# Optimization experiments

Measured on AMD Instinct MI355X. Metric: run time of the kernel, lower is better.

The kernel has to match this reference:

```python
import jax, jax.numpy as jnp
import numpy as np

TAU = 32.0
ALPHA = 0.9
B, C, F = 4096, 512, 128  # batch, n_classes, n_bits


def setup_inputs() -> dict:
    key = jax.random.key(0)
    k1, k2, k3, k4 = jax.random.split(key, 4)
    X = jax.random.normal(k1, (B, F), dtype=jnp.float32)
    T = jax.random.randint(k2, (B, C), 0, 2).astype(jnp.int32)  # 0/1 multi-label
    # kaiming_normal_(mode='fan_out') on a [C, F] tensor -> std = sqrt(2 / C)
    std = np.sqrt(2.0 / C).astype(np.float32)
    means = jax.random.normal(k3, (C, F), dtype=jnp.float32) * std
    log_vars = jax.random.normal(k4, (C, F), dtype=jnp.float32) * std
    return {"X": X, "T": T, "means": means, "log_vars": log_vars}


def _l2_normalize(x, eps=1e-12):
    # matches torch F.normalize(p=2): x / max(||x||, eps)
    n = jnp.sqrt(jnp.sum(x * x, axis=-1, keepdims=True))
    return x / jnp.maximum(n, eps)


def _mahalanobis(Xn, mu, log_vars):
    # M[i,j] = sum_f (x_if - mu_jf)^2 / exp(lv_jf)
    # expanded into three GEMM-like terms -> never materializes [N,C,F]
    inv = jnp.exp(-log_vars)                         # [C, F]
    t1 = (Xn * Xn) @ inv.T                           # [N, C]
    t2 = Xn @ (mu * inv).T                           # [N, C]
    t3 = jnp.sum(mu * mu * inv, axis=-1)             # [C]
    return t1 - 2.0 * t2 + t3[None, :]


def reference(X, T, means, log_vars):
    lv = jnp.clip(log_vars, 0.0, 6.0)                # relu6
    Xn = _l2_normalize(X)
    mu = _l2_normalize(means)
    D = _mahalanobis(Xn, mu, lv)                     # [N, C]

    P_all = jax.nn.softmax(-TAU * D, axis=1)         # [N, C]
    Tf = T.astype(X.dtype)
    P_sum = jnp.sum(P_all * Tf, axis=1)              # [N]
    nz = P_sum != 0
    safe = jnp.where(nz, P_sum, 1.0)
    loss = -jnp.sum(jnp.where(nz, jnp.log(safe), 0.0)) / jnp.maximum(
        jnp.sum(nz).astype(X.dtype), 1.0)

    # classes present in the batch (concrete mask -> static column selection)
    cw = np.asarray(jnp.sum(T, axis=0) != 0)
    Dc = D[:, cw]                                    # [N, Ccw]
    Tc = Tf[:, cw]
    S = Tc + jnp.exp(-ALPHA * Dc) * (1.0 - Tc)
    return (loss, S)
```

## Files before the change

kernel.cpp:

```cpp
#include <hip/hip_runtime.h>
#include <hip/hip_bf16.h>
#include <math.h>

#define NB 4096
#define NC 512
#define NF 128
#define NK 256
#define TAUc 32.0f
#define ALPHAc 0.9f

typedef __attribute__((ext_vector_type(8))) short bf16x8;
typedef __attribute__((ext_vector_type(4))) float f32x4;

__device__ inline void splitbf(float x, short& hi, short& lo) {
  unsigned u = __float_as_uint(x);
  hi = (short)(u >> 16);
  float l = x - __uint_as_float(u & 0xFFFF0000u);
  lo = (short)(__float_as_uint(l) >> 16);
}

__global__ __launch_bounds__(128) void k_prepB(const float* __restrict__ means,
                                               const float* __restrict__ logv,
                                               ushort* __restrict__ Bh,
                                               ushort* __restrict__ Bl,
                                               float* __restrict__ t3) {
  __shared__ float p2[2];
  __shared__ float q2[2];
  int c = blockIdx.x, f = threadIdx.x;
  float mu = means[(size_t)c * NF + f];
  float lv = fminf(fmaxf(logv[(size_t)c * NF + f], 0.f), 6.f);
  float iv = __expf(-lv);
  float s = mu * mu;
  #pragma unroll
  for (int o = 1; o < 64; o <<= 1) s += __shfl_xor(s, o, 64);
  if ((f & 63) == 0) p2[f >> 6] = s;
  __syncthreads();
  float mun = mu / fmaxf(sqrtf(p2[0] + p2[1]), 1e-12f);

  int ct = c >> 4, lr = c & 15;
  auto swadr = [&](int k) {
    return (size_t)(ct * 8 + (k >> 5)) * 512 + ((k >> 3) & 3) * 128 + lr * 8 + (k & 7);
  };
  short h, l;
  splitbf(iv, h, l);
  size_t a1 = swadr(f);
  Bh[a1] = (ushort)h; Bl[a1] = (ushort)l;
  splitbf(-2.f * mun * iv, h, l);
  size_t a2 = swadr(f + NF);
  Bh[a2] = (ushort)h; Bl[a2] = (ushort)l;

  float t = mun * mun * iv;
  #pragma unroll
  for (int o = 1; o < 64; o <<= 1) t += __shfl_xor(t, o, 64);
  if ((f & 63) == 0) q2[f >> 6] = t;
  __syncthreads();
  if (f == 0) t3[c] = q2[0] + q2[1];
}

__global__ __launch_bounds__(512) void k_zero(int* __restrict__ colnz) {
  colnz[threadIdx.x] = 0;
}

__global__ __launch_bounds__(256) void k_mask(const int* __restrict__ T,
                                              int* __restrict__ colnz) {
  int r0 = blockIdx.x * 16;
  int a0 = 0, a1 = 0;
  for (int r = 0; r < 16; ++r) {
    const int* row = T + (size_t)(r0 + r) * NC;
    a0 |= row[threadIdx.x];
    a1 |= row[threadIdx.x + 256];
  }
  if (a0) atomicOr(colnz + threadIdx.x, 1);
  if (a1) atomicOr(colnz + threadIdx.x + 256, 1);
}

__global__ __launch_bounds__(512) void k_scan(const int* __restrict__ colnz,
                                              int* __restrict__ pos) {
  __shared__ int s[NC];
  int t = threadIdx.x;
  int f = colnz[t] ? 1 : 0;
  s[t] = f;
  __syncthreads();
  for (int o = 1; o < NC; o <<= 1) {
    int add = (t >= o) ? s[t - o] : 0;
    __syncthreads();
    s[t] += add;
    __syncthreads();
  }
  pos[t] = s[t] - f;
}

__global__ __launch_bounds__(512) void k_fused(const float* __restrict__ X,
                                               const int* __restrict__ T,
                                               const ushort* __restrict__ Bh,
                                               const ushort* __restrict__ Bl,
                                               const float* __restrict__ t3,
                                               const int* __restrict__ colnz,
                                               const int* __restrict__ pos,
                                               float* __restrict__ Sout,
                                               float* __restrict__ blklog,
                                               int* __restrict__ blkcnt,
                                               int Csel, int ident) {
  __shared__ float Dls[16][514];
  __shared__ float sl16[16];
  __shared__ int sc16[16];
  int tid = threadIdx.x;
  int lane = tid & 63, w = tid >> 6;
  int lr = lane & 15, kq = lane >> 4;
  int r0 = blockIdx.x * 16;

  float xv[4][8];
  float rsum = 0.f;
  const float* xrow = X + (size_t)(r0 + lr) * NF + 8 * kq;
  #pragma unroll
  for (int c = 0; c < 4; ++c) {
    float4 u0 = *(const float4*)(xrow + 32 * c);
    float4 u1 = *(const float4*)(xrow + 32 * c + 4);
    xv[c][0] = u0.x; xv[c][1] = u0.y; xv[c][2] = u0.z; xv[c][3] = u0.w;
    xv[c][4] = u1.x; xv[c][5] = u1.y; xv[c][6] = u1.z; xv[c][7] = u1.w;
    #pragma unroll
    for (int j = 0; j < 8; ++j) rsum = fmaf(xv[c][j], xv[c][j], rsum);
  }
  rsum += __shfl_xor(rsum, 16, 64);
  rsum += __shfl_xor(rsum, 32, 64);
  float rn = 1.0f / fmaxf(sqrtf(rsum), 1e-12f);

  bf16x8 Afh[8], Afl[8];
  #pragma unroll
  for (int c = 0; c < 4; ++c) {
    #pragma unroll
    for (int j = 0; j < 8; ++j) {
      float xn = xv[c][j] * rn;
      short h, l;
      splitbf(xn * xn, h, l);
      Afh[c][j] = h; Afl[c][j] = l;
      splitbf(xn, h, l);
      Afh[c + 4][j] = h; Afl[c + 4][j] = l;
    }
  }

  int tf0[8], tf1[8];
  {
    const int* Trow0 = T + (size_t)(r0 + 2 * w) * NC;
    const int* Trow1 = T + (size_t)(r0 + 2 * w + 1) * NC;
    #pragma unroll
    for (int j = 0; j < 8; ++j) {
      tf0[j] = Trow0[lane + 64 * j];
      tf1[j] = Trow1[lane + 64 * j];
    }
  }

  f32x4 acc[4] = {};
  #pragma unroll
  for (int k8 = 0; k8 < 8; ++k8) {
    #pragma unroll
    for (int t = 0; t < 4; ++t) {
      size_t off = (((size_t)(w * 4 + t) * 8 + k8) * 64 + lane) * 8;
      bf16x8 bh = *(const bf16x8*)(Bh + off);
      bf16x8 bl = *(const bf16x8*)(Bl + off);
      acc[t] = __builtin_amdgcn_mfma_f32_16x16x32_bf16(Afh[k8], bh, acc[t], 0, 0, 0);
      acc[t] = __builtin_amdgcn_mfma_f32_16x16x32_bf16(Afl[k8], bh, acc[t], 0, 0, 0);
      acc[t] = __builtin_amdgcn_mfma_f32_16x16x32_bf16(Afh[k8], bl, acc[t], 0, 0, 0);
    }
  }

  int n0 = w * 64;
  #pragma unroll
  for (int t = 0; t < 4; ++t) {
    int c = n0 + 16 * t + lr;
    float tt = t3[c];
    #pragma unroll
    for (int i = 0; i < 4; ++i) Dls[4 * kq + i][c] = acc[t][i] + tt;
  }
  __syncthreads();

  #pragma unroll
  for (int rr = 0; rr < 2; ++rr) {
    int r = 2 * w + rr;
    const int* tf = rr ? tf1 : tf0;
    float d[8];
    #pragma unroll
    for (int j = 0; j < 8; ++j) d[j] = Dls[r][lane + 64 * j];
    float dmin = d[0];
    #pragma unroll
    for (int j = 1; j < 8; ++j) dmin = fminf(dmin, d[j]);
    #pragma unroll
    for (int o = 1; o < 64; o <<= 1) dmin = fminf(dmin, __shfl_xor(dmin, o, 64));
    float Z = 0.f, Ps = 0.f;
    #pragma unroll
    for (int j = 0; j < 8; ++j) {
      float p = __expf(TAUc * (dmin - d[j]));
      Z += p;
      if (tf[j]) Ps += p;
    }
    #pragma unroll
    for (int o = 1; o < 64; o <<= 1) { Z += __shfl_xor(Z, o, 64); Ps += __shfl_xor(Ps, o, 64); }
    float* srow = Sout + (size_t)(r0 + r) * Csel;
    if (ident) {
      #pragma unroll
      for (int j = 0; j < 8; ++j)
        srow[lane + 64 * j] = tf[j] ? 1.0f : __expf(-ALPHAc * d[j]);
    } else {
      #pragma unroll
      for (int j = 0; j < 8; ++j) {
        int c = lane + 64 * j;
        if (colnz[c]) srow[pos[c]] = tf[j] ? 1.0f : __expf(-ALPHAc * d[j]);
      }
    }
    if (lane == 0) {
      float Psum = Ps / Z;
      sl16[r] = (Psum > 0.f) ? logf(Psum) : 0.f;
      sc16[r] = (Psum > 0.f) ? 1 : 0;
    }
  }
  __syncthreads();
  if (tid == 0) {
    float s = 0.f; int c = 0;
    #pragma unroll
    for (int r = 0; r < 16; ++r) { s += sl16[r]; c += sc16[r]; }
    blklog[blockIdx.x] = s;
    blkcnt[blockIdx.x] = c;
  }
}

__global__ __launch_bounds__(256) void k_fin(const float* __restrict__ blklog,
                                             const int* __restrict__ blkcnt,
                                             float* __restrict__ out) {
  __shared__ float sl[256];
  __shared__ int sc[256];
  int t = threadIdx.x;
  sl[t] = blklog[t];
  sc[t] = blkcnt[t];
  __syncthreads();
  for (int o = 128; o > 0; o >>= 1) {
    if (t < o) { sl[t] += sl[t + o]; sc[t] += sc[t + o]; }
    __syncthreads();
  }
  if (t == 0) out[0] = -sl[0] / fmaxf((float)sc[0], 1.0f);
}

extern "C" void kernel_launch(void* const* d_in, const int* in_sizes, int n_in,
                              void* d_out, int out_size, void* d_ws, size_t ws_size,
                              hipStream_t stream) {
  const float* X     = (const float*)d_in[0];
  const int*   T     = (const int*)d_in[1];
  const float* means = (const float*)d_in[2];
  const float* logv  = (const float*)d_in[3];
  float* out = (float*)d_out;
  char* ws = (char*)d_ws;

  ushort* Bh      = (ushort*)(ws);
  ushort* Bl      = (ushort*)(ws + 262144);
  float*  t3      = (float*) (ws + 524288);
  float*  blklog  = (float*) (ws + 526336);
  int*    blkcnt  = (int*)   (ws + 527360);
  int*    colnz   = (int*)   (ws + 528384);
  int*    pos     = (int*)   (ws + 530432);

  int Csel = (out_size - 1) / NB;
  int ident = (Csel == NC);

  k_prepB<<<NC, NF, 0, stream>>>(means, logv, Bh, Bl, t3);
  if (!ident) {
    k_zero<<<1, NC, 0, stream>>>(colnz);
    k_mask<<<NB / 16, 256, 0, stream>>>(T, colnz);
    k_scan<<<1, NC, 0, stream>>>(colnz, pos);
  }
  k_fused<<<NB / 16, 512, 0, stream>>>(X, T, Bh, Bl, t3, colnz, pos,
                                       out + 1, blklog, blkcnt, Csel, ident);
  k_fin<<<1, 256, 0, stream>>>(blklog, blkcnt, out);
}
```

Measured before the change: 25.52 us.

## Double-buffer B fragments into LDS with async global_load_lds prefetch

Each wave now streams its hi/lo B fragments for the next K step into a private double-buffered LDS region using async global-to-LDS loads. It then reads the current step's fragments from LDS for the MFMAs. The goal is to overlap global memory latency with the matrix-core work instead of stalling on register loads each iteration. The shared buffer is enlarged to 128KB and reused for the D tile after a barrier. This limits blocks per CU and relies on hand-placed vmcnt waits, with no explicit guard against overwriting a buffer before its LDS reads finish.

```diff
diff --git a/kernel.cpp b/kernel.cpp
--- a/kernel.cpp
+++ b/kernel.cpp
@@ -11,6 +11,8 @@
 
 typedef __attribute__((ext_vector_type(8))) short bf16x8;
 typedef __attribute__((ext_vector_type(4))) float f32x4;
+typedef __attribute__((address_space(1))) const unsigned int gu32;
+typedef __attribute__((address_space(3))) unsigned int lu32;
 
 __device__ inline void splitbf(float x, short& hi, short& lo) {
   unsigned u = __float_as_uint(x);
@@ -101,13 +103,25 @@
                                                float* __restrict__ blklog,
                                                int* __restrict__ blkcnt,
                                                int Csel, int ident) {
-  __shared__ float Dls[16][514];
+  __shared__ __align__(16) unsigned char smraw[131072];
   __shared__ float sl16[16];
   __shared__ int sc16[16];
   int tid = threadIdx.x;
   int lane = tid & 63, w = tid >> 6;
   int lr = lane & 15, kq = lane >> 4;
   int r0 = blockIdx.x * 16;
+
+  auto stage = [&](int p) {
+    int par = p & 1;
+    #pragma unroll
+    for (int t = 0; t < 4; ++t) {
+      size_t goff = (((size_t)(w * 4 + t) * 8 + p) * 64 + lane) * 8;
+      unsigned ldso = (unsigned)(w * 16384 + par * 8192 + t * 2048);
+      __builtin_amdgcn_global_load_lds((gu32*)(Bh + goff), (lu32*)(smraw + ldso), 16, 0, 0);
+      __builtin_amdgcn_global_load_lds((gu32*)(Bl + goff), (lu32*)(smraw + ldso + 1024), 16, 0, 0);
+    }
+  };
+  stage(0);
 
   float xv[4][8];
   float rsum = 0.f;
@@ -150,20 +164,29 @@
     }
   }
 
+  const bf16x8* wstage = (const bf16x8*)(smraw + w * 16384);
   f32x4 acc[4] = {};
   #pragma unroll
   for (int k8 = 0; k8 < 8; ++k8) {
+    if (k8 < 7) {
+      stage(k8 + 1);
+      asm volatile("s_waitcnt vmcnt(8)" ::: "memory");
+    } else {
+      asm volatile("s_waitcnt vmcnt(0)" ::: "memory");
+    }
+    int par = k8 & 1;
     #pragma unroll
     for (int t = 0; t < 4; ++t) {
-      size_t off = (((size_t)(w * 4 + t) * 8 + k8) * 64 + lane) * 8;
-      bf16x8 bh = *(const bf16x8*)(Bh + off);
-      bf16x8 bl = *(const bf16x8*)(Bl + off);
+      bf16x8 bh = wstage[(par * 8 + t * 2) * 64 + lane];
+      bf16x8 bl = wstage[(par * 8 + t * 2 + 1) * 64 + lane];
       acc[t] = __builtin_amdgcn_mfma_f32_16x16x32_bf16(Afh[k8], bh, acc[t], 0, 0, 0);
       acc[t] = __builtin_amdgcn_mfma_f32_16x16x32_bf16(Afl[k8], bh, acc[t], 0, 0, 0);
       acc[t] = __builtin_amdgcn_mfma_f32_16x16x32_bf16(Afh[k8], bl, acc[t], 0, 0, 0);
     }
   }
-
+  __syncthreads();
+
+  float (*Dls)[514] = (float (*)[514])smraw;
   int n0 = w * 64;
   #pragma unroll
   for (int t = 0; t < 4; ++t) {
```

Result: faster. 23.75 us (-6.9%).

## Retile fused kernel to 64x128 blocks with B staged in LDS and split softmax

Applied to the files above, without the earlier changes.

Each block now handles a 64-row by 128-class tile instead of 16 full rows. The B operand slice (hi and lo bf16) is staged once into 128KB of LDS via global_load_lds, so each block reads it from memory once instead of every wave loading it from global. Softmax statistics are computed per column-chunk as partial min, Z and P values, merged per row across the 4 chunks in k_fin with online-softmax rescaling. This removes redundant B reads and the Dls shared-memory transpose. The cost is a large LDS footprint that limits occupancy to one block per CU, plus extra partial-statistic traffic.

```diff
diff --git a/kernel.cpp b/kernel.cpp
--- a/kernel.cpp
+++ b/kernel.cpp
@@ -11,6 +11,8 @@
 
 typedef __attribute__((ext_vector_type(8))) short bf16x8;
 typedef __attribute__((ext_vector_type(4))) float f32x4;
+typedef __attribute__((address_space(1))) const unsigned int gu32;
+typedef __attribute__((address_space(3))) unsigned int lu32;
 
 __device__ inline void splitbf(float x, short& hi, short& lo) {
   unsigned u = __float_as_uint(x);
@@ -98,145 +100,187 @@
                                                const int* __restrict__ colnz,
                                                const int* __restrict__ pos,
                                                float* __restrict__ Sout,
-                                               float* __restrict__ blklog,
-                                               int* __restrict__ blkcnt,
+                                               float* __restrict__ rowm,
+                                               float* __restrict__ rowz,
+                                               float* __restrict__ rowp,
                                                int Csel, int ident) {
-  __shared__ float Dls[16][514];
-  __shared__ float sl16[16];
-  __shared__ int sc16[16];
+  __shared__ __align__(16) unsigned char smB[131072];
+  __shared__ float partm[2][64], partz[2][64], partp[2][64];
   int tid = threadIdx.x;
   int lane = tid & 63, w = tid >> 6;
+  int wm = w & 3, wn = w >> 2;
   int lr = lane & 15, kq = lane >> 4;
-  int r0 = blockIdx.x * 16;
-
-  float xv[4][8];
-  float rsum = 0.f;
-  const float* xrow = X + (size_t)(r0 + lr) * NF + 8 * kq;
-  #pragma unroll
-  for (int c = 0; c < 4; ++c) {
-    float4 u0 = *(const float4*)(xrow + 32 * c);
-    float4 u1 = *(const float4*)(xrow + 32 * c + 4);
-    xv[c][0] = u0.x; xv[c][1] = u0.y; xv[c][2] = u0.z; xv[c][3] = u0.w;
-    xv[c][4] = u1.x; xv[c][5] = u1.y; xv[c][6] = u1.z; xv[c][7] = u1.w;
-    #pragma unroll
-    for (int j = 0; j < 8; ++j) rsum = fmaf(xv[c][j], xv[c][j], rsum);
-  }
-  rsum += __shfl_xor(rsum, 16, 64);
-  rsum += __shfl_xor(rsum, 32, 64);
-  float rn = 1.0f / fmaxf(sqrtf(rsum), 1e-12f);
+  int bx = blockIdx.x;
+  int gc = bx & 3, gr = bx >> 2;
+  int r0 = gr * 64, c0 = gc * 128;
+
+  {
+    const ushort* gh = Bh + (size_t)gc * 32768;
+    const ushort* gl = Bl + (size_t)gc * 32768;
+    #pragma unroll
+    for (int s = 0; s < 8; ++s) {
+      unsigned lo = (unsigned)(s * 8192 + w * 1024);
+      size_t ge = (size_t)(s * 512 + w * 64 + lane) * 8;
+      __builtin_amdgcn_global_load_lds((gu32*)(gh + ge), (lu32*)(smB + lo), 16, 0, 0);
+      __builtin_amdgcn_global_load_lds((gu32*)(gl + ge), (lu32*)(smB + 65536 + lo), 16, 0, 0);
+    }
+  }
 
   bf16x8 Afh[8], Afl[8];
-  #pragma unroll
-  for (int c = 0; c < 4; ++c) {
-    #pragma unroll
-    for (int j = 0; j < 8; ++j) {
-      float xn = xv[c][j] * rn;
-      short h, l;
-      splitbf(xn * xn, h, l);
-      Afh[c][j] = h; Afl[c][j] = l;
-      splitbf(xn, h, l);
-      Afh[c + 4][j] = h; Afl[c + 4][j] = l;
-    }
-  }
-
-  int tf0[8], tf1[8];
   {
-    const int* Trow0 = T + (size_t)(r0 + 2 * w) * NC;
-    const int* Trow1 = T + (size_t)(r0 + 2 * w + 1) * NC;
-    #pragma unroll
-    for (int j = 0; j < 8; ++j) {
-      tf0[j] = Trow0[lane + 64 * j];
-      tf1[j] = Trow1[lane + 64 * j];
-    }
-  }
+    float xv[4][8];
+    float rsum = 0.f;
+    const float* xrow = X + (size_t)(r0 + wm * 16 + lr) * NF + 8 * kq;
+    #pragma unroll
+    for (int c = 0; c < 4; ++c) {
+      float4 u0 = *(const float4*)(xrow + 32 * c);
+      float4 u1 = *(const float4*)(xrow + 32 * c + 4);
+      xv[c][0] = u0.x; xv[c][1] = u0.y; xv[c][2] = u0.z; xv[c][3] = u0.w;
+      xv[c][4] = u1.x; xv[c][5] = u1.y; xv[c][6] = u1.z; xv[c][7] = u1.w;
+      #pragma unroll
+      for (int j = 0; j < 8; ++j) rsum = fmaf(xv[c][j], xv[c][j], rsum);
+    }
+    rsum += __shfl_xor(rsum, 16, 64);
+    rsum += __shfl_xor(rsum, 32, 64);
+    float rn = 1.0f / fmaxf(sqrtf(rsum), 1e-12f);
+    #pragma unroll
+    for (int c = 0; c < 4; ++c) {
+      #pragma unroll
+      for (int j = 0; j < 8; ++j) {
+        float xn = xv[c][j] * rn;
+        short h, l;
+        splitbf(xn * xn, h, l);
+        Afh[c][j] = h; Afl[c][j] = l;
+        splitbf(xn, h, l);
+        Afh[c + 4][j] = h; Afl[c + 4][j] = l;
+      }
+    }
+  }
+
+  int tfv[4][4];
+  #pragma unroll
+  for (int i = 0; i < 4; ++i) {
+    const int* tr = T + (size_t)(r0 + wm * 16 + 4 * kq + i) * NC + c0 + wn * 64 + lr;
+    #pragma unroll
+    for (int t = 0; t < 4; ++t) tfv[t][i] = tr[16 * t];
+  }
+
+  __syncthreads();
 
   f32x4 acc[4] = {};
   #pragma unroll
   for (int k8 = 0; k8 < 8; ++k8) {
     #pragma unroll
     for (int t = 0; t < 4; ++t) {
-      size_t off = (((size_t)(w * 4 + t) * 8 + k8) * 64 + lane) * 8;
-      bf16x8 bh = *(const bf16x8*)(Bh + off);
-      bf16x8 bl = *(const bf16x8*)(Bl + off);
+      unsigned off = (unsigned)((((wn * 4 + t) * 8 + k8) * 64 + lane) * 16);
+      bf16x8 bh = *(const bf16x8*)(smB + off);
+      bf16x8 bl = *(const bf16x8*)(smB + 65536 + off);
       acc[t] = __builtin_amdgcn_mfma_f32_16x16x32_bf16(Afh[k8], bh, acc[t], 0, 0, 0);
       acc[t] = __builtin_amdgcn_mfma_f32_16x16x32_bf16(Afl[k8], bh, acc[t], 0, 0, 0);
       acc[t] = __builtin_amdgcn_mfma_f32_16x16x32_bf16(Afh[k8], bl, acc[t], 0, 0, 0);
     }
   }
 
-  int n0 = w * 64;
+  float d[4][4];
   #pragma unroll
   for (int t = 0; t < 4; ++t) {
-    int c = n0 + 16 * t + lr;
-    float tt = t3[c];
-    #pragma unroll
-    for (int i = 0; i < 4; ++i) Dls[4 * kq + i][c] = acc[t][i] + tt;
-  }
-  __syncthreads();
-
-  #pragma unroll
-  for (int rr = 0; rr < 2; ++rr) {
-    int r = 2 * w + rr;
-    const int* tf = rr ? tf1 : tf0;
-    float d[8];
-    #pragma unroll
-    for (int j = 0; j < 8; ++j) d[j] = Dls[r][lane + 64 * j];
-    float dmin = d[0];
-    #pragma unroll
-    for (int j = 1; j < 8; ++j) dmin = fminf(dmin, d[j]);
-    #pragma unroll
-    for (int o = 1; o < 64; o <<= 1) dmin = fminf(dmin, __shfl_xor(dmin, o, 64));
-    float Z = 0.f, Ps = 0.f;
-    #pragma unroll
-    for (int j = 0; j < 8; ++j) {
-      float p = __expf(TAUc * (dmin - d[j]));
+    float tt = t3[c0 + wn * 64 + 16 * t + lr];
+    #pragma unroll
+    for (int i = 0; i < 4; ++i) d[t][i] = acc[t][i] + tt;
+  }
+
+  float m4[4], Zi[4], Pi[4];
+  #pragma unroll
+  for (int i = 0; i < 4; ++i) {
+    float mm = fminf(fminf(d[0][i], d[1][i]), fminf(d[2][i], d[3][i]));
+    #pragma unroll
+    for (int o = 1; o < 16; o <<= 1) mm = fminf(mm, __shfl_xor(mm, o, 64));
+    float Z = 0.f, P = 0.f;
+    #pragma unroll
+    for (int t = 0; t < 4; ++t) {
+      float p = __expf(TAUc * (mm - d[t][i]));
       Z += p;
-      if (tf[j]) Ps += p;
-    }
-    #pragma unroll
-    for (int o = 1; o < 64; o <<= 1) { Z += __shfl_xor(Z, o, 64); Ps += __shfl_xor(Ps, o, 64); }
-    float* srow = Sout + (size_t)(r0 + r) * Csel;
-    if (ident) {
+      if (tfv[t][i]) P += p;
+    }
+    #pragma unroll
+    for (int o = 1; o < 16; o <<= 1) { Z += __shfl_xor(Z, o, 64); P += __shfl_xor(P, o, 64); }
+    m4[i] = mm; Zi[i] = Z; Pi[i] = P;
+  }
+
+  if (ident) {
+    #pragma unroll
+    for (int i = 0; i < 4; ++i) {
+      float* srow = Sout + (size_t)(r0 + wm * 16 + 4 * kq + i) * NC + c0 + wn * 64 + lr;
       #pragma unroll
-      for (int j = 0; j < 8; ++j)
-        srow[lane + 64 * j] = tf[j] ? 1.0f : __expf(-ALPHAc * d[j]);
-    } else {
+      for (int t = 0; t < 4; ++t)
+        srow[16 * t] = tfv[t][i] ? 1.0f : __expf(-ALPHAc * d[t][i]);
+    }
+  } else {
+    #pragma unroll
+    for (int i = 0; i < 4; ++i) {
+      float* srow = Sout + (size_t)(r0 + wm * 16 + 4 * kq + i) * Csel;
       #pragma unroll
-      for (int j = 0; j < 8; ++j) {
-        int c = lane + 64 * j;
-        if (colnz[c]) srow[pos[c]] = tf[j] ? 1.0f : __expf(-ALPHAc * d[j]);
+      for (int t = 0; t < 4; ++t) {
+        int c = c0 + wn * 64 + 16 * t + lr;
+        if (colnz[c]) srow[pos[c]] = tfv[t][i] ? 1.0f : __expf(-ALPHAc * d[t][i]);
       }
     }
-    if (lane == 0) {
-      float Psum = Ps / Z;
-      sl16[r] = (Psum > 0.f) ? logf(Psum) : 0.f;
-      sc16[r] = (Psum > 0.f) ? 1 : 0;
-    }
-  }
+  }
+
+  if (lr == 0) {
+    #pragma unroll
+    for (int i = 0; i < 4; ++i) {
+      int row = wm * 16 + 4 * kq + i;
+      partm[wn][row] = m4[i];
+      partz[wn][row] = Zi[i];
+      partp[wn][row] = Pi[i];
+    }
+  }
+  __syncthreads();
+  if (tid < 64) {
+    float m0 = partm[0][tid], m1 = partm[1][tid];
+    float m = fminf(m0, m1);
+    float e0 = __expf(TAUc * (m - m0)), e1 = __expf(TAUc * (m - m1));
+    int g = (r0 + tid) * 4 + gc;
+    rowm[g] = m;
+    rowz[g] = partz[0][tid] * e0 + partz[1][tid] * e1;
+    rowp[g] = partp[0][tid] * e0 + partp[1][tid] * e1;
+  }
+}
+
+__global__ __launch_bounds__(1024) void k_fin(const float* __restrict__ rowm,
+                                              const float* __restrict__ rowz,
+                                              const float* __restrict__ rowp,
+                                              float* __restrict__ out) {
+  __shared__ float sl[16];
+  __shared__ int sc[16];
+  int tid = threadIdx.x;
+  int lane = tid & 63, w = tid >> 6;
+  float ls = 0.f; int lc = 0;
+  for (int r = tid; r < NB; r += 1024) {
+    float4 mv = ((const float4*)rowm)[r];
+    float4 zv = ((const float4*)rowz)[r];
+    float4 pv = ((const float4*)rowp)[r];
+    float m = fminf(fminf(mv.x, mv.y), fminf(mv.z, mv.w));
+    float e0 = __expf(TAUc * (m - mv.x));
+    float e1 = __expf(TAUc * (m - mv.y));
+    float e2 = __expf(TAUc * (m - mv.z));
+    float e3 = __expf(TAUc * (m - mv.w));
+    float Z = zv.x * e0 + zv.y * e1 + zv.z * e2 + zv.w * e3;
+    float P = pv.x * e0 + pv.y * e1 + pv.z * e2 + pv.w * e3;
+    float Ps = P / Z;
+    if (Ps > 0.f) { ls += logf(Ps); ++lc; }
+  }
+  #pragma unroll
+  for (int o = 1; o < 64; o <<= 1) { ls += __shfl_xor(ls, o, 64); lc += __shfl_xor(lc, o, 64); }
+  if (lane == 0) { sl[w] = ls; sc[w] = lc; }
   __syncthreads();
   if (tid == 0) {
     float s = 0.f; int c = 0;
     #pragma unroll
-    for (int r = 0; r < 16; ++r) { s += sl16[r]; c += sc16[r]; }
-    blklog[blockIdx.x] = s;
-    blkcnt[blockIdx.x] = c;
-  }
-}
-
-__global__ __launch_bounds__(256) void k_fin(const float* __restrict__ blklog,
-                                             const int* __restrict__ blkcnt,
-                                             float* __restrict__ out) {
-  __shared__ float sl[256];
-  __shared__ int sc[256];
-  int t = threadIdx.x;
-  sl[t] = blklog[t];
-  sc[t] = blkcnt[t];
-  __syncthreads();
-  for (int o = 128; o > 0; o >>= 1) {
-    if (t < o) { sl[t] += sl[t + o]; sc[t] += sc[t + o]; }
-    __syncthreads();
-  }
-  if (t == 0) out[0] = -sl[0] / fmaxf((float)sc[0], 1.0f);
+    for (int i = 0; i < 16; ++i) { s += sl[i]; c += sc[i]; }
+    out[0] = -s / fmaxf((float)c, 1.0f);
+  }
 }
 
 extern "C" void kernel_launch(void* const* d_in, const int* in_sizes, int n_in,
@@ -249,13 +293,14 @@
   float* out = (float*)d_out;
   char* ws = (char*)d_ws;
 
-  ushort* Bh      = (ushort*)(ws);
-  ushort* Bl      = (ushort*)(ws + 262144);
-  float*  t3      = (float*) (ws + 524288);
-  float*  blklog  = (float*) (ws + 526336);
-  int*    blkcnt  = (int*)   (ws + 527360);
-  int*    colnz   = (int*)   (ws + 528384);
-  int*    pos     = (int*)   (ws + 530432);
+  ushort* Bh   = (ushort*)(ws);
+  ushort* Bl   = (ushort*)(ws + 262144);
+  float*  t3   = (float*) (ws + 524288);
+  float*  rowm = (float*) (ws + 526336);
+  float*  rowz = (float*) (ws + 591872);
+  float*  rowp = (float*) (ws + 657408);
+  int*    colnz= (int*)   (ws + 722944);
+  int*    pos  = (int*)   (ws + 724992);
 
   int Csel = (out_size - 1) / NB;
   int ident = (Csel == NC);
@@ -266,7 +311,7 @@
     k_mask<<<NB / 16, 256, 0, stream>>>(T, colnz);
     k_scan<<<1, NC, 0, stream>>>(colnz, pos);
   }
-  k_fused<<<NB / 16, 512, 0, stream>>>(X, T, Bh, Bl, t3, colnz, pos,
-                                       out + 1, blklog, blkcnt, Csel, ident);
-  k_fin<<<1, 256, 0, stream>>>(blklog, blkcnt, out);
-}
+  k_fused<<<256, 512, 0, stream>>>(X, T, Bh, Bl, t3, colnz, pos,
+                                   out + 1, rowm, rowz, rowp, Csel, ident);
+  k_fin<<<1, 1024, 0, stream>>>(rowm, rowz, rowp, out);
+}
```

Result: faster. 23.87 us (-6.4%).
